# Kernel tuning notes

Hardware: AMD Instinct MI355X
Metric: run time of the kernel (lower is better)

## Reference

```python
import jax, jax.numpy as jnp
import numpy as np

N_QUBITS = 12
DIM = 1 << N_QUBITS
W_MUL = (2.0 ** 0.5) * (5.0 ** -0.5)  # he_std * lrmul with gain=sqrt(2), lrmul=1


def _pair_gates(thetas):
    """thetas: [P,3] angles (rxx, ryy, rzz) -> [P,4,4] gate Rzz@Ryy@Rxx per pair."""
    c = jnp.cos(thetas / 2).astype(jnp.complex64)
    s = jnp.sin(thetas / 2).astype(jnp.complex64)
    I4 = jnp.eye(4, dtype=jnp.complex64)
    X = jnp.array([[0, 1], [1, 0]], jnp.complex64)
    Y = jnp.array([[0, -1j], [1j, 0]], jnp.complex64)
    Z = jnp.array([[1, 0], [0, -1]], jnp.complex64)
    XX, YY, ZZ = jnp.kron(X, X), jnp.kron(Y, Y), jnp.kron(Z, Z)
    rot = lambda cc, ss, P: cc[:, None, None] * I4 - 1j * ss[:, None, None] * P
    Rxx = rot(c[:, 0], s[:, 0], XX)
    Ryy = rot(c[:, 1], s[:, 1], YY)
    Rzz = rot(c[:, 2], s[:, 2], ZZ)
    # circuit applies rxx, then ryy, then rzz -> U_pair = Rzz @ Ryy @ Rxx
    return jnp.einsum('pij,pjk,pkl->pil', Rzz, Ryy, Rxx)


def _build_U(weight):
    n = N_QUBITS
    w = weight * W_MUL
    # i = 3*n + 3*which_q for which_q in 0,2,...,n-2 (as in qconv0)
    idx = 3 * n + 3 * np.arange(0, n, 2)
    thetas = jnp.stack([w[idx], w[idx + 1], w[idx + 2]], axis=-1)  # [n/2, 3]
    G = _pair_gates(thetas)
    U = G[0]
    for p in range(1, n // 2):  # qubit 0 is the most-significant leg
        U = jnp.kron(U, G[p])
    return U  # [DIM, DIM]


def setup_inputs() -> dict:
    key = jax.random.key(0)
    kx, kw = jax.random.split(key)
    x = jax.random.normal(kx, (2, 1, DIM), dtype=jnp.float32)
    x = x / jnp.linalg.norm(x, axis=-1, keepdims=True)  # normalized quantum states
    weight = jax.random.uniform(kw, (6 * N_QUBITS,), dtype=jnp.float32,
                                minval=0.0, maxval=2 * np.pi)
    return {"x": x, "weight": weight, "dimA": N_QUBITS // 2}


def reference(x, weight, dimA):
    n, dim = N_QUBITS, DIM
    B = x.shape[0]
    psi = x.astype(jnp.complex64)[:, 0, :]                    # [B, dim]
    rho = jnp.einsum('bi,bj->bij', psi, jnp.conj(psi))        # rho = psi psi^dagger
    U = _build_U(weight)
    rho2 = jnp.einsum('ij,bjk,lk->bil', U, rho, jnp.conj(U))  # U rho U^dagger
    dimB = n - dimA
    dB, dA = 1 << dimB, 1 << dimA
    # partial trace over leading dimB qubits (trace_lst = range(dimB))
    red = jnp.einsum('btitj->bij', rho2.reshape(B, dB, dA, dB, dA))
    return red.reshape(B, 1, dA * dA)  # dA*dA == dim since dimA = n/2
```

## Files before the change

### kernel.cpp

```cpp
#include <hip/hip_runtime.h>

#define DIMQ 4096
#define NPAIR 6
#define DA 64

__device__ __forceinline__ float2 cmul(float2 a, float2 b) {
    return make_float2(a.x*b.x - a.y*b.y, a.x*b.y + a.y*b.x);
}
__device__ __forceinline__ float2 cfma2(float2 a, float2 u, float2 b, float2 v) {
    return make_float2(a.x*u.x - a.y*u.y + b.x*v.x - b.y*v.y,
                       a.x*u.y + a.y*u.x + b.x*v.y + b.y*v.x);
}

__global__ __launch_bounds__(1024) void quconv_kernel(
    const float* __restrict__ x,
    const float* __restrict__ w,
    float* __restrict__ out,
    int real_only)
{
    __shared__ float2 buf[DIMQ];
    __shared__ float2 G[NPAIR][4];

    const int tid = threadIdx.x;
    const int b   = blockIdx.x >> 2;
    const int s   = blockIdx.x & 3;

    if (tid < NPAIR) {
        const float WM = 0.63245553203367586640f;
        const int base = 36 + 6 * tid;
        const float tx = 0.5f * WM * w[base + 0];
        const float ty = 0.5f * WM * w[base + 1];
        const float tz = 0.5f * WM * w[base + 2];
        float cm, sm, cp, sp, cz, sz;
        __sincosf(tx - ty, &sm, &cm);
        __sincosf(tx + ty, &sp, &cp);
        __sincosf(tz,      &sz, &cz);
        const float2 em = make_float2(cz, -sz);
        const float2 ep = make_float2(cz,  sz);
        G[tid][0] = make_float2(cz * cm, -sz * cm);
        G[tid][1] = cmul(em, make_float2(0.f, -sm));
        G[tid][2] = make_float2(cz * cp,  sz * cp);
        G[tid][3] = cmul(ep, make_float2(0.f, -sp));
    }

    {
        const float4 v = ((const float4*)(x + b * DIMQ))[tid];
        buf[tid * 4 + 0] = make_float2(v.x, 0.f);
        buf[tid * 4 + 1] = make_float2(v.y, 0.f);
        buf[tid * 4 + 2] = make_float2(v.z, 0.f);
        buf[tid * 4 + 3] = make_float2(v.w, 0.f);
    }

    for (int p = 0; p < NPAIR; ++p) {
        __syncthreads();
        const int shift = 2 * (5 - p);
        const int g = tid;
        const int low  = g & ((1 << shift) - 1);
        const int base = ((g >> shift) << (shift + 2)) | low;
        const int s1 = 1 << shift;
        const float2 A = G[p][0], B = G[p][1], C = G[p][2], D = G[p][3];
        const float2 v0 = buf[base];
        const float2 v1 = buf[base + s1];
        const float2 v2 = buf[base + 2 * s1];
        const float2 v3 = buf[base + 3 * s1];
        buf[base]          = cfma2(A, v0, B, v3);
        buf[base + s1]     = cfma2(C, v1, D, v2);
        buf[base + 2 * s1] = cfma2(D, v1, C, v2);
        buf[base + 3 * s1] = cfma2(B, v0, A, v3);
    }
    __syncthreads();

    const int i = (s << 4) + (tid >> 6);
    const int j = tid & 63;
    float re = 0.f, im = 0.f;
    #pragma unroll 8
    for (int t = 0; t < 64; ++t) {
        const float2 pi = buf[t * DA + i];
        const float2 pj = buf[t * DA + j];
        re += pi.x * pj.x + pi.y * pj.y;
        im += pi.y * pj.x - pi.x * pj.y;
    }
    const int e = b * (DA * DA) + i * DA + j;
    if (real_only) {
        out[e] = re;
    } else {
        ((float2*)out)[e] = make_float2(re, im);
    }
}

extern "C" void kernel_launch(void* const* d_in, const int* in_sizes, int n_in,
                              void* d_out, int out_size, void* d_ws, size_t ws_size,
                              hipStream_t stream) {
    const float* x = (const float*)d_in[0];
    const float* w = (const float*)d_in[1];
    const int B = in_sizes[0] / DIMQ;
    const int real_only = (out_size == B * DA * DA) ? 1 : 0;
    quconv_kernel<<<dim3(B * 4), dim3(1024), 0, stream>>>(x, w, (float*)d_out, real_only);
}
```

Before: 62.95 us.

## Exploit partial trace to skip traced-out gates and apply subsystem unitary to reduced matrix

Instead of evolving the full 4096-element state through all six pair gates and then tracing, the kernel computes the real reduced density matrix X X^T directly from the input (the gates on the traced-out qubits cancel) and then applies only the three kept-subsystem pair gates as U rho U^dagger. The right multiplication uses wave shuffles, and the left multiplication combines eight rows through a small shared exchange buffer. Blocks shrink to 512 threads and there are eight per batch, so the input is staged transposed in shared memory. This drops the per-block full state evolution and its repeated barriers, at the cost of more intricate index logic.

```diff
diff --git a/kernel.cpp b/kernel.cpp
--- a/kernel.cpp
+++ b/kernel.cpp
@@ -1,33 +1,32 @@
 #include <hip/hip_runtime.h>
 
 #define DIMQ 4096
-#define NPAIR 6
 #define DA 64
+#define LST 66
 
 __device__ __forceinline__ float2 cmul(float2 a, float2 b) {
     return make_float2(a.x*b.x - a.y*b.y, a.x*b.y + a.y*b.x);
 }
-__device__ __forceinline__ float2 cfma2(float2 a, float2 u, float2 b, float2 v) {
-    return make_float2(a.x*u.x - a.y*u.y + b.x*v.x - b.y*v.y,
-                       a.x*u.y + a.y*u.x + b.x*v.y + b.y*v.x);
-}
+__device__ __forceinline__ float2 conjf2(float2 a) { return make_float2(a.x, -a.y); }
 
-__global__ __launch_bounds__(1024) void quconv_kernel(
+__global__ __launch_bounds__(512) void quconv_kernel(
     const float* __restrict__ x,
     const float* __restrict__ w,
     float* __restrict__ out,
     int real_only)
 {
-    __shared__ float2 buf[DIMQ];
-    __shared__ float2 G[NPAIR][4];
+    __shared__ float  Xt[DA][LST];
+    __shared__ float2 exch[8][DA + 1];
+    __shared__ float2 G[3][4];
 
     const int tid = threadIdx.x;
-    const int b   = blockIdx.x >> 2;
-    const int s   = blockIdx.x & 3;
+    const int b   = blockIdx.x >> 3;
+    const int o   = blockIdx.x & 7;
 
-    if (tid < NPAIR) {
+    if (tid < 3) {
+        const int k = tid;
         const float WM = 0.63245553203367586640f;
-        const int base = 36 + 6 * tid;
+        const int base = 54 + 6 * (2 - k);
         const float tx = 0.5f * WM * w[base + 0];
         const float ty = 0.5f * WM * w[base + 1];
         const float tz = 0.5f * WM * w[base + 2];
@@ -35,56 +34,85 @@
         __sincosf(tx - ty, &sm, &cm);
         __sincosf(tx + ty, &sp, &cp);
         __sincosf(tz,      &sz, &cz);
-        const float2 em = make_float2(cz, -sz);
-        const float2 ep = make_float2(cz,  sz);
-        G[tid][0] = make_float2(cz * cm, -sz * cm);
-        G[tid][1] = cmul(em, make_float2(0.f, -sm));
-        G[tid][2] = make_float2(cz * cp,  sz * cp);
-        G[tid][3] = cmul(ep, make_float2(0.f, -sp));
+        G[k][0] = make_float2(cz * cm, -sz * cm);
+        G[k][1] = cmul(make_float2(cz, -sz), make_float2(0.f, -sm));
+        G[k][2] = make_float2(cz * cp,  sz * cp);
+        G[k][3] = cmul(make_float2(cz,  sz), make_float2(0.f, -sp));
     }
 
+    const int m = tid >> 6;
+    const int j = tid & 63;
+
     {
-        const float4 v = ((const float4*)(x + b * DIMQ))[tid];
-        buf[tid * 4 + 0] = make_float2(v.x, 0.f);
-        buf[tid * 4 + 1] = make_float2(v.y, 0.f);
-        buf[tid * 4 + 2] = make_float2(v.z, 0.f);
-        buf[tid * 4 + 3] = make_float2(v.w, 0.f);
-    }
-
-    for (int p = 0; p < NPAIR; ++p) {
-        __syncthreads();
-        const int shift = 2 * (5 - p);
-        const int g = tid;
-        const int low  = g & ((1 << shift) - 1);
-        const int base = ((g >> shift) << (shift + 2)) | low;
-        const int s1 = 1 << shift;
-        const float2 A = G[p][0], B = G[p][1], C = G[p][2], D = G[p][3];
-        const float2 v0 = buf[base];
-        const float2 v1 = buf[base + s1];
-        const float2 v2 = buf[base + 2 * s1];
-        const float2 v3 = buf[base + 3 * s1];
-        buf[base]          = cfma2(A, v0, B, v3);
-        buf[base + s1]     = cfma2(C, v1, D, v2);
-        buf[base + 2 * s1] = cfma2(D, v1, C, v2);
-        buf[base + 3 * s1] = cfma2(B, v0, A, v3);
+        float v[8];
+        #pragma unroll
+        for (int q = 0; q < 8; ++q)
+            v[q] = x[b * DIMQ + (m * 8 + q) * DA + j];
+        #pragma unroll
+        for (int q = 0; q < 8; q += 2)
+            *(float2*)&Xt[j][m * 8 + q] = make_float2(v[q], v[q + 1]);
     }
     __syncthreads();
 
-    const int i = (s << 4) + (tid >> 6);
-    const int j = tid & 63;
-    float re = 0.f, im = 0.f;
-    #pragma unroll 8
-    for (int t = 0; t < 64; ++t) {
-        const float2 pi = buf[t * DA + i];
-        const float2 pj = buf[t * DA + j];
-        re += pi.x * pj.x + pi.y * pj.y;
-        im += pi.y * pj.x - pi.x * pj.y;
+    int r = 0;
+    #pragma unroll
+    for (int k = 0; k < 3; ++k) {
+        const int bk = (o >> k) & 1;
+        const int mk = (m >> k) & 1;
+        const int d  = bk ? (mk ? 2 : 1) : (mk ? 3 : 0);
+        r += d << (2 * k);
     }
-    const int e = b * (DA * DA) + i * DA + j;
+
+    float acc = 0.f;
+    {
+        const float* xr = Xt[r];
+        const float* xj = Xt[j];
+        #pragma unroll
+        for (int t = 0; t < DA; t += 2) {
+            const float2 a = *(const float2*)&xr[t];
+            const float2 c = *(const float2*)&xj[t];
+            acc += a.x * c.x + a.y * c.y;
+        }
+    }
+    float2 v = make_float2(acc, 0.f);
+
+    #pragma unroll
+    for (int k = 2; k >= 0; --k) {
+        const int mask = 3 << (2 * k);
+        const int d    = (j >> (2 * k)) & 3;
+        const bool mid = (d == 1) || (d == 2);
+        const float2 P = conjf2(mid ? G[k][2] : G[k][0]);
+        const float2 Q = conjf2(mid ? G[k][3] : G[k][1]);
+        const float2 vp = make_float2(__shfl_xor(v.x, mask), __shfl_xor(v.y, mask));
+        const float2 t1 = cmul(P, v);
+        const float2 t2 = cmul(Q, vp);
+        v = make_float2(t1.x + t2.x, t1.y + t2.y);
+    }
+
+    exch[m][j] = v;
+    __syncthreads();
+    float2 res = make_float2(0.f, 0.f);
+    #pragma unroll
+    for (int mp = 0; mp < 8; ++mp) {
+        float2 cf = make_float2(1.f, 0.f);
+        #pragma unroll
+        for (int k = 0; k < 3; ++k) {
+            const int bk    = (o >> k) & 1;
+            const bool flip = ((m ^ mp) >> k) & 1;
+            const float2 g  = flip ? (bk ? G[k][3] : G[k][1])
+                                   : (bk ? G[k][2] : G[k][0]);
+            cf = cmul(cf, g);
+        }
+        const float2 nv = exch[mp][j];
+        res.x += cf.x * nv.x - cf.y * nv.y;
+        res.y += cf.x * nv.y + cf.y * nv.x;
+    }
+
+    const int e = b * (DA * DA) + r * DA + j;
     if (real_only) {
-        out[e] = re;
+        out[e] = res.x;
     } else {
-        ((float2*)out)[e] = make_float2(re, im);
+        ((float2*)out)[e] = res;
     }
 }
 
@@ -95,5 +123,5 @@
     const float* w = (const float*)d_in[1];
     const int B = in_sizes[0] / DIMQ;
     const int real_only = (out_size == B * DA * DA) ? 1 : 0;
-    quconv_kernel<<<dim3(B * 4), dim3(1024), 0, stream>>>(x, w, (float*)d_out, real_only);
+    quconv_kernel<<<dim3(B * 8), dim3(512), 0, stream>>>(x, w, (float*)d_out, real_only);
 }
```

Result: faster. 58.74 us (-6.7%).
